# Kernel optimization log

Hardware: AMD Instinct MI355X
Metric: run time of the kernel (lower is better)

## Reference

```python
import jax, jax.numpy as jnp
import numpy as np
from jax import lax

B, KLEN, KDIM, QDIM, ADIM, VDIM = 32, 2000, 512, 512, 512, 512
CONV_CH, CONV_K = 10, 201

def setup_inputs() -> dict:
    key = jax.random.key(0)
    ks = jax.random.split(key, 16)
    s = lambda fan: 1.0 / np.sqrt(fan)
    return {
        "key": jax.random.normal(ks[0], (B, KLEN, KDIM), jnp.float32),
        "value": jax.random.normal(ks[1], (B, KLEN, VDIM), jnp.float32),
        "query": jax.random.normal(ks[2], (B, 1, QDIM), jnp.float32),
        "aw_prev": jnp.zeros((B, 1, KLEN), jnp.float32),
        "mask": jnp.ones((B, 1, KLEN), jnp.int32),
        # parameters (torch nn.Linear: y = x @ W.T + b, W is [out,in])
        "Wk": jax.random.uniform(ks[3], (ADIM, KDIM), jnp.float32, -s(KDIM), s(KDIM)),
        "bk": jax.random.uniform(ks[4], (ADIM,), jnp.float32, -s(KDIM), s(KDIM)),
        "Wq": jax.random.uniform(ks[5], (ADIM, QDIM), jnp.float32, -s(QDIM), s(QDIM)),
        "conv_w": jax.random.uniform(ks[6], (CONV_CH, 1, CONV_K), jnp.float32, -s(CONV_K), s(CONV_K)),
        "Wconv": jax.random.uniform(ks[7], (ADIM, CONV_CH), jnp.float32, -s(CONV_CH), s(CONV_CH)),
        "v": jax.random.uniform(ks[8], (ADIM,), jnp.float32, -s(ADIM), s(ADIM)),
    }

def reference(key, value, query, aw_prev, mask, Wk, bk, Wq, conv_w, Wconv, v):
    # location-aware attention, qlen == 1, sharpening_factor == 1, no dropout (eval)
    kproj = jnp.einsum('bkd,ad->bka', key, Wk) + bk              # [B, klen, adim]
    qproj = jnp.einsum('bqd,ad->bqa', query, Wq)                 # [B, 1, adim]
    # conv over previous attention weights: 1D 'same' conv, 1 -> CONV_CH channels
    conv_feat = lax.conv_general_dilated(
        aw_prev, conv_w, window_strides=(1,), padding='SAME',
        dimension_numbers=('NCH', 'OIH', 'NCH'))                 # [B, C, klen]
    conv_proj = jnp.einsum('bck,ac->bka', conv_feat, Wconv)      # [B, klen, adim]
    # additive score: v^T tanh(Wk k + Wq q + Wc f)
    tmp = jnp.tanh(kproj[:, None] + qproj[:, :, None] + conv_proj[:, None])  # [B,1,klen,adim]
    e = jnp.einsum('bqka,a->bqk', tmp, v)                        # [B, 1, klen]
    neg_inf = jnp.finfo(e.dtype).min
    e = jnp.where(mask == 0, neg_inf, e)
    aw = jax.nn.softmax(e, axis=-1)                              # [B, 1, klen]
    cv = jnp.einsum('bqk,bkv->bqv', aw, value)                   # [B, 1, vdim]
    return cv, aw[:, None]  # aw: [B, 1(H), 1(qlen), klen]
```

## Files before the change

### kernel.cpp

```cpp
#include <hip/hip_runtime.h>
#include <hip/hip_bf16.h>
#include <math.h>

#define B 32
#define KLEN 2000
#define KDIM 512
#define QDIM 512
#define ADIM 512
#define VDIM 512
#define CONV_CH 10
#define CONV_K 201
#define NROWS (B*KLEN)

#define NKS  33
#define ZERO16 {0,0,0,0,0,0,0,0,0,0,0,0,0,0,0,0}

#define NP_PACK 53
#define NP_QPRJ 26
#define NP_ZERO 26
#define NP_CONV 256

#define CH_LEN 63

typedef __attribute__((ext_vector_type(8)))  short bf16x8;
typedef __attribute__((ext_vector_type(16))) float f32x16;
typedef __attribute__((ext_vector_type(4)))  float f32x4;

__device__ __forceinline__ ushort f32_to_bf16(float f) {
    union { float f; unsigned int u; } v; v.f = f;
    unsigned int x = v.u;
    unsigned int r = (x + 0x7FFFu + ((x >> 16) & 1u)) >> 16;
    return (ushort)r;
}

__device__ __forceinline__ unsigned int pk_bf16(float lo, float hi) {
    union { __hip_bfloat162 h2; unsigned int u; } c;
    float2 t; t.x = lo; t.y = hi;
    c.h2 = __float22bfloat162_rn(t);
    return c.u;
}

__device__ __forceinline__ float fast_tanh(float x) {
    return 1.0f - 2.0f / (__expf(2.0f * x) + 1.0f);
}

#define MFMA32(a, bfr, c) __builtin_amdgcn_mfma_f32_32x32x16_bf16(a, bfr, c, 0, 0, 0)

__global__ __launch_bounds__(640, 2)
void k_prep(const float* __restrict__ Wk, const float* __restrict__ Wconv,
            const float* __restrict__ bk, ushort* __restrict__ wp,
            const float* __restrict__ query, const float* __restrict__ Wq,
            float* __restrict__ qproj,
            const float* __restrict__ aw_prev, const float* __restrict__ conv_w,
            float* __restrict__ cf, float* __restrict__ cv) {
    __shared__ float w_s[CONV_CH * 204];
    __shared__ float aw_s[464];
    const int bid = blockIdx.x, tid = threadIdx.x;

    if (bid < NP_PACK) {
        int t = bid * 640 + tid;
        if (t < 16 * NKS * 64) {
            int lane = t & 63;
            int idx = t >> 6;
            int ks = idx % NKS, nt = idx / NKS;
            int h = lane >> 5, r = lane & 31;
            int a = nt * 32 + r;
            int j0 = ks * 16 + h * 8;
            union { uint4 v; ushort u[8]; } pk;
            #pragma unroll
            for (int jj = 0; jj < 8; jj++) {
                int j = j0 + jj;
                float val;
                if (j < 512)       val = Wk[a * KDIM + j];
                else if (j < 522)  val = Wconv[a * CONV_CH + (j - 512)];
                else if (j == 522) val = bk[a];
                else               val = 0.f;
                pk.u[jj] = f32_to_bf16(val);
            }
            *(uint4*)(wp + (size_t)t * 8) = pk.v;
        }
    } else if (bid < NP_PACK + NP_QPRJ) {
        int t = (bid - NP_PACK) * 640 + tid;
        if (t < B * ADIM) {
            int b = t >> 9, a = t & 511;
            const f32x4* q = (const f32x4*)(query + b * QDIM);
            const f32x4* w = (const f32x4*)(Wq + a * QDIM);
            float acc = 0.f;
            #pragma unroll 4
            for (int i = 0; i < 128; i++) {
                f32x4 qv = q[i], wv = w[i];
                acc += qv[0]*wv[0] + qv[1]*wv[1] + qv[2]*wv[2] + qv[3]*wv[3];
            }
            qproj[t] = acc;
        }
    } else if (bid < NP_PACK + NP_QPRJ + NP_ZERO) {
        int t = (bid - NP_PACK - NP_QPRJ) * 640 + tid;
        if (t < B * VDIM) cv[t] = 0.f;
    } else {
        int cb = bid - NP_PACK - NP_QPRJ - NP_ZERO;
        int b = cb >> 3, chunk = cb & 7;
        int k0 = chunk * 256;
        for (int i = tid; i < CONV_CH * 204; i += 640) {
            int c = i / 204, t = i % 204;
            w_s[i] = (t < CONV_K) ? conv_w[c * CONV_K + t] : 0.f;
        }
        for (int i = tid; i < 464; i += 640) {
            int src = k0 - 100 + i;
            aw_s[i] = (src >= 0 && src < KLEN) ? aw_prev[b * KLEN + src] : 0.f;
        }
        __syncthreads();

        const int c = tid >> 6;
        const int k_local = (tid & 63) * 4;
        const float* wc = w_s + c * 204;
        float a0 = 0.f, a1 = 0.f, a2 = 0.f, a3 = 0.f;
        f32x4 r0 = *(const f32x4*)(aw_s + k_local);
        #pragma unroll 3
        for (int q = 0; q < 51; q++) {
            f32x4 r1 = *(const f32x4*)(aw_s + k_local + 4 * q + 4);
            float w0 = wc[4*q], w1 = wc[4*q+1], w2 = wc[4*q+2], w3 = wc[4*q+3];
            a0 += w0*r0[0]; a1 += w0*r0[1]; a2 += w0*r0[2]; a3 += w0*r0[3];
            a0 += w1*r0[1]; a1 += w1*r0[2]; a2 += w1*r0[3]; a3 += w1*r1[0];
            a0 += w2*r0[2]; a1 += w2*r0[3]; a2 += w2*r1[0]; a3 += w2*r1[1];
            a0 += w3*r0[3]; a1 += w3*r1[0]; a2 += w3*r1[1]; a3 += w3*r1[2];
            r0 = r1;
        }
        int k = k0 + k_local;
        float* dst = cf + ((size_t)b * CONV_CH + c) * KLEN + k;
        if (k + 3 < KLEN) {
            f32x4 o; o[0] = a0; o[1] = a1; o[2] = a2; o[3] = a3;
            *(f32x4*)dst = o;
        } else {
            if (k     < KLEN) dst[0] = a0;
            if (k + 1 < KLEN) dst[1] = a1;
            if (k + 2 < KLEN) dst[2] = a2;
            if (k + 3 < KLEN) dst[3] = a3;
        }
    }
}

__global__ __launch_bounds__(512, 4)
void k_main(const float* __restrict__ key, const ushort* __restrict__ wp,
            const float* __restrict__ qproj, const float* __restrict__ cf,
            const float* __restrict__ vvec, const int* __restrict__ mask,
            float* __restrict__ e_out) {
    __shared__ char Alds[65536];
    __shared__ float partsum[8][2][32];
    const int tid = threadIdx.x;
    const int wc = tid >> 6, lane = tid & 63;
    const int r = lane & 31, h = lane >> 5;
    const int b = blockIdx.x >> 5;
    const int kbase = (blockIdx.x & 31) * 64;

    #pragma unroll
    for (int i = 0; i < 8; i++) {
        int ch = tid + i * 512;
        int arow = ch >> 6, cx = ch & 63;
        int kpos = kbase + arow; if (kpos >= KLEN) kpos = KLEN - 1;
        const float* kp = key + ((size_t)b * KLEN + kpos) * KDIM + cx * 8;
        f32x4 f0 = __builtin_nontemporal_load((const f32x4*)kp);
        f32x4 f1 = __builtin_nontemporal_load((const f32x4*)(kp + 4));
        uint4 pk;
        pk.x = pk_bf16(f0[0], f0[1]);
        pk.y = pk_bf16(f0[2], f0[3]);
        pk.z = pk_bf16(f1[0], f1[1]);
        pk.w = pk_bf16(f1[2], f1[3]);
        int off = (arow << 10) + (cx << 4);
        off ^= (arow & 31) << 4;
        *(uint4*)(Alds + off) = pk;
    }
    __syncthreads();

    const ushort* bpW0 = wp + ((size_t)(wc * 2 + 0) * NKS * 64 + lane) * 8;
    const ushort* bpW1 = wp + ((size_t)(wc * 2 + 1) * NKS * 64 + lane) * 8;
    const int base_g0 = r * 1024 + h * 16;
    const int base_g1 = base_g0 + 32768;
    const int swz = r << 4;

    f32x16 c00 = ZERO16, c01 = ZERO16;
    f32x16 c10 = ZERO16, c11 = ZERO16;

    #pragma unroll 4
    for (int ks = 0; ks < 32; ks++) {
        bf16x8 k0 = *(const bf16x8*)(Alds + ((base_g0 + ks * 32) ^ swz));
        bf16x8 k1 = *(const bf16x8*)(Alds + ((base_g1 + ks * 32) ^ swz));
        bf16x8 w0 = *(const bf16x8*)(bpW0 + ks * 512);
        bf16x8 w1 = *(const bf16x8*)(bpW1 + ks * 512);
        c00 = MFMA32(w0, k0, c00); c01 = MFMA32(w0, k1, c01);
        c10 = MFMA32(w1, k0, c10); c11 = MFMA32(w1, k1, c11);
    }
    {
        auto build_ext = [&](int kpos) -> bf16x8 {
            int kc = kpos < KLEN ? kpos : KLEN - 1;
            const float* cfb = cf + ((size_t)b * CONV_CH) * KLEN + kc;
            union { bf16x8 v8; unsigned int u[4]; ushort us[8]; } pk;
            if (h == 0) {
                pk.u[0] = pk_bf16(cfb[0],              cfb[(size_t)1 * KLEN]);
                pk.u[1] = pk_bf16(cfb[(size_t)2*KLEN], cfb[(size_t)3 * KLEN]);
                pk.u[2] = pk_bf16(cfb[(size_t)4*KLEN], cfb[(size_t)5 * KLEN]);
                pk.u[3] = pk_bf16(cfb[(size_t)6*KLEN], cfb[(size_t)7 * KLEN]);
            } else {
                pk.u[0] = pk_bf16(cfb[(size_t)8*KLEN], cfb[(size_t)9 * KLEN]);
                pk.us[2] = 0x3F80;
                pk.us[3] = 0;
                pk.u[2] = 0; pk.u[3] = 0;
            }
            return pk.v8;
        };
        bf16x8 x0 = build_ext(kbase + r);
        bf16x8 x1 = build_ext(kbase + 32 + r);
        bf16x8 w0 = *(const bf16x8*)(bpW0 + 32 * 512);
        bf16x8 w1 = *(const bf16x8*)(bpW1 + 32 * 512);
        c00 = MFMA32(w0, x0, c00); c01 = MFMA32(w0, x1, c01);
        c10 = MFMA32(w1, x0, c10); c11 = MFMA32(w1, x1, c11);
    }

    const float* qb = qproj + b * ADIM + wc * 64;
    const float* vb = vvec + wc * 64;
    float pg0 = 0.f, pg1 = 0.f;
    #pragma unroll
    for (int t = 0; t < 2; t++) {
        const f32x16 a0 = t ? c10 : c00;
        const f32x16 a1 = t ? c11 : c01;
        #pragma unroll
        for (int q = 0; q < 4; q++) {
            f32x4 qv = *(const f32x4*)(qb + t * 32 + 8 * q + 4 * h);
            f32x4 vv = *(const f32x4*)(vb + t * 32 + 8 * q + 4 * h);
            #pragma unroll
            for (int j = 0; j < 4; j++) {
                int i = 4 * q + j;
                pg0 += fast_tanh(a0[i] + qv[j]) * vv[j];
                pg1 += fast_tanh(a1[i] + qv[j]) * vv[j];
            }
        }
    }
    pg0 += __shfl_xor(pg0, 32);
    pg1 += __shfl_xor(pg1, 32);
    if (h == 0) { partsum[wc][0][r] = pg0; partsum[wc][1][r] = pg1; }
    __syncthreads();

    if (tid < 64) {
        int g = tid >> 5, rr = tid & 31;
        float s = 0.f;
        #pragma unroll
        for (int w = 0; w < 8; w++) s += partsum[w][g][rr];
        int kpos = kbase + g * 32 + rr;
        if (kpos < KLEN) {
            int idx = b * KLEN + kpos;
            e_out[idx] = mask[idx] ? s : -3.4028235e38f;
        }
    }
}

__global__ __launch_bounds__(512, 4)
void k_cv(const float* __restrict__ e, const float* __restrict__ value,
          float* __restrict__ aw, float* __restrict__ cv) {
    int b = blockIdx.x >> 5, chunk = blockIdx.x & 31;
    const float* er = e + b * KLEN;
    __shared__ float redv[8];
    __shared__ float sa[CH_LEN + 1];
    __shared__ f32x4 red[3][128];
    int tid = threadIdx.x, lane = tid & 63, wv = tid >> 6;

    float m = -3.4028235e38f;
    for (int k = tid; k < KLEN; k += 512) m = fmaxf(m, er[k]);
    for (int o = 32; o; o >>= 1) m = fmaxf(m, __shfl_xor(m, o));
    if (lane == 0) redv[wv] = m;
    __syncthreads();
    m = fmaxf(fmaxf(fmaxf(redv[0], redv[1]), fmaxf(redv[2], redv[3])),
              fmaxf(fmaxf(redv[4], redv[5]), fmaxf(redv[6], redv[7])));
    __syncthreads();
    float s = 0.f;
    for (int k = tid; k < KLEN; k += 512) s += __expf(er[k] - m);
    for (int o = 32; o; o >>= 1) s += __shfl_xor(s, o);
    if (lane == 0) redv[wv] = s;
    __syncthreads();
    s = redv[0] + redv[1] + redv[2] + redv[3] + redv[4] + redv[5] + redv[6] + redv[7];
    const float inv = 1.0f / s;

    int k0 = chunk * CH_LEN;
    int len = KLEN - k0; if (len > CH_LEN) len = CH_LEN;
    if (tid < len) {
        float p = __expf(er[k0 + tid] - m) * inv;
        sa[tid] = p;
        aw[b * KLEN + k0 + tid] = p;
    }
    __syncthreads();

    const int kh = tid >> 7;
    const int colt = tid & 127;
    const float* vp = value + ((size_t)b * KLEN + k0) * VDIM + colt * 4;
    f32x4 acc = {0.f, 0.f, 0.f, 0.f};
    for (int k = kh; k < len; k += 4) {
        f32x4 vv = *(const f32x4*)(vp + (size_t)k * VDIM);
        acc += vv * sa[k];
    }
    if (kh) red[kh - 1][colt] = acc;
    __syncthreads();
    if (kh == 0) {
        acc += red[0][colt] + red[1][colt] + red[2][colt];
        float* dst = cv + b * VDIM + colt * 4;
        atomicAdd(dst + 0, acc[0]);
        atomicAdd(dst + 1, acc[1]);
        atomicAdd(dst + 2, acc[2]);
        atomicAdd(dst + 3, acc[3]);
    }
}

extern "C" void kernel_launch(void* const* d_in, const int* in_sizes, int n_in,
                              void* d_out, int out_size, void* d_ws, size_t ws_size,
                              hipStream_t stream) {
    const float* key     = (const float*)d_in[0];
    const float* value   = (const float*)d_in[1];
    const float* query   = (const float*)d_in[2];
    const float* aw_prev = (const float*)d_in[3];
    const int*   mask    = (const int*)d_in[4];
    const float* Wk      = (const float*)d_in[5];
    const float* bk      = (const float*)d_in[6];
    const float* Wq      = (const float*)d_in[7];
    const float* conv_w  = (const float*)d_in[8];
    const float* Wconv   = (const float*)d_in[9];
    const float* vvec    = (const float*)d_in[10];

    char* ws = (char*)d_ws;
    ushort* wp   = (ushort*)(ws + 0);
    float* qproj = (float*)(ws + 540672);
    float* cf    = (float*)(ws + 606208);
    float* e     = (float*)(ws + 3166208);

    float* cv = (float*)d_out;
    float* aw = (float*)d_out + B * VDIM;

    k_prep<<<NP_PACK + NP_QPRJ + NP_ZERO + NP_CONV, 640, 0, stream>>>(
              Wk, Wconv, bk, wp, query, Wq, qproj, aw_prev, conv_w, cf, cv);
    k_main<<<1024, 512, 0, stream>>>(key, wp, qproj, cf, vvec, mask, e);
    k_cv  <<<B*32, 512, 0, stream>>>(e, value, aw, cv);
}
```

Measured before the change: 140.2 us.

## Double k_main row tile to 128 keys per block to reuse weight fragments

```diff
diff --git a/kernel.cpp b/kernel.cpp
--- a/kernel.cpp
+++ b/kernel.cpp
@@ -139,27 +139,26 @@
     }
 }
 
-__global__ __launch_bounds__(512, 4)
+__global__ __launch_bounds__(512, 2)
 void k_main(const float* __restrict__ key, const ushort* __restrict__ wp,
             const float* __restrict__ qproj, const float* __restrict__ cf,
             const float* __restrict__ vvec, const int* __restrict__ mask,
             float* __restrict__ e_out) {
-    __shared__ char Alds[65536];
-    __shared__ float partsum[8][2][32];
+    __shared__ char Alds[131072];
     const int tid = threadIdx.x;
     const int wc = tid >> 6, lane = tid & 63;
     const int r = lane & 31, h = lane >> 5;
-    const int b = blockIdx.x >> 5;
-    const int kbase = (blockIdx.x & 31) * 64;
+    const int b = blockIdx.x >> 4;
+    const int kbase = (blockIdx.x & 15) * 128;
 
     #pragma unroll
-    for (int i = 0; i < 8; i++) {
+    for (int i = 0; i < 16; i++) {
         int ch = tid + i * 512;
         int arow = ch >> 6, cx = ch & 63;
         int kpos = kbase + arow; if (kpos >= KLEN) kpos = KLEN - 1;
         const float* kp = key + ((size_t)b * KLEN + kpos) * KDIM + cx * 8;
-        f32x4 f0 = __builtin_nontemporal_load((const f32x4*)kp);
-        f32x4 f1 = __builtin_nontemporal_load((const f32x4*)(kp + 4));
+        f32x4 f0 = *(const f32x4*)kp;
+        f32x4 f1 = *(const f32x4*)(kp + 4);
         uint4 pk;
         pk.x = pk_bf16(f0[0], f0[1]);
         pk.y = pk_bf16(f0[2], f0[3]);
@@ -173,21 +172,26 @@
 
     const ushort* bpW0 = wp + ((size_t)(wc * 2 + 0) * NKS * 64 + lane) * 8;
     const ushort* bpW1 = wp + ((size_t)(wc * 2 + 1) * NKS * 64 + lane) * 8;
-    const int base_g0 = r * 1024 + h * 16;
-    const int base_g1 = base_g0 + 32768;
+    const int koff = r * 1024 + h * 16;
     const int swz = r << 4;
 
     f32x16 c00 = ZERO16, c01 = ZERO16;
     f32x16 c10 = ZERO16, c11 = ZERO16;
-
-    #pragma unroll 4
+    f32x16 c20 = ZERO16, c21 = ZERO16;
+    f32x16 c30 = ZERO16, c31 = ZERO16;
+
+    #pragma unroll 2
     for (int ks = 0; ks < 32; ks++) {
-        bf16x8 k0 = *(const bf16x8*)(Alds + ((base_g0 + ks * 32) ^ swz));
-        bf16x8 k1 = *(const bf16x8*)(Alds + ((base_g1 + ks * 32) ^ swz));
+        bf16x8 k0 = *(const bf16x8*)(Alds + ((koff          + ks * 32) ^ swz));
+        bf16x8 k1 = *(const bf16x8*)(Alds + ((koff + 32768  + ks * 32) ^ swz));
+        bf16x8 k2 = *(const bf16x8*)(Alds + ((koff + 65536  + ks * 32) ^ swz));
+        bf16x8 k3 = *(const bf16x8*)(Alds + ((koff + 98304  + ks * 32) ^ swz));
         bf16x8 w0 = *(const bf16x8*)(bpW0 + ks * 512);
         bf16x8 w1 = *(const bf16x8*)(bpW1 + ks * 512);
-        c00 = MFMA32(w0, k0, c00); c01 = MFMA32(w0, k1, c01);
-        c10 = MFMA32(w1, k0, c10); c11 = MFMA32(w1, k1, c11);
+        c00 = MFMA32(w0, k0, c00); c10 = MFMA32(w0, k1, c10);
+        c20 = MFMA32(w0, k2, c20); c30 = MFMA32(w0, k3, c30);
+        c01 = MFMA32(w1, k0, c01); c11 = MFMA32(w1, k1, c11);
+        c21 = MFMA32(w1, k2, c21); c31 = MFMA32(w1, k3, c31);
     }
     {
         auto build_ext = [&](int kpos) -> bf16x8 {
@@ -209,41 +213,54 @@
         };
         bf16x8 x0 = build_ext(kbase + r);
         bf16x8 x1 = build_ext(kbase + 32 + r);
+        bf16x8 x2 = build_ext(kbase + 64 + r);
+        bf16x8 x3 = build_ext(kbase + 96 + r);
         bf16x8 w0 = *(const bf16x8*)(bpW0 + 32 * 512);
         bf16x8 w1 = *(const bf16x8*)(bpW1 + 32 * 512);
-        c00 = MFMA32(w0, x0, c00); c01 = MFMA32(w0, x1, c01);
-        c10 = MFMA32(w1, x0, c10); c11 = MFMA32(w1, x1, c11);
+        c00 = MFMA32(w0, x0, c00); c10 = MFMA32(w0, x1, c10);
+        c20 = MFMA32(w0, x2, c20); c30 = MFMA32(w0, x3, c30);
+        c01 = MFMA32(w1, x0, c01); c11 = MFMA32(w1, x1, c11);
+        c21 = MFMA32(w1, x2, c21); c31 = MFMA32(w1, x3, c31);
     }
 
     const float* qb = qproj + b * ADIM + wc * 64;
     const float* vb = vvec + wc * 64;
-    float pg0 = 0.f, pg1 = 0.f;
+    float pg0 = 0.f, pg1 = 0.f, pg2 = 0.f, pg3 = 0.f;
     #pragma unroll
-    for (int t = 0; t < 2; t++) {
-        const f32x16 a0 = t ? c10 : c00;
-        const f32x16 a1 = t ? c11 : c01;
+    for (int q = 0; q < 4; q++) {
+        f32x4 qv0 = *(const f32x4*)(qb + 8 * q + 4 * h);
+        f32x4 vv0 = *(const f32x4*)(vb + 8 * q + 4 * h);
+        f32x4 qv1 = *(const f32x4*)(qb + 32 + 8 * q + 4 * h);
+        f32x4 vv1 = *(const f32x4*)(vb + 32 + 8 * q + 4 * h);
         #pragma unroll
-        for (int q = 0; q < 4; q++) {
-            f32x4 qv = *(const f32x4*)(qb + t * 32 + 8 * q + 4 * h);
-            f32x4 vv = *(const f32x4*)(vb + t * 32 + 8 * q + 4 * h);
-            #pragma unroll
-            for (int j = 0; j < 4; j++) {
-                int i = 4 * q + j;
-                pg0 += fast_tanh(a0[i] + qv[j]) * vv[j];
-                pg1 += fast_tanh(a1[i] + qv[j]) * vv[j];
-            }
+        for (int j = 0; j < 4; j++) {
+            int i = 4 * q + j;
+            pg0 += fast_tanh(c00[i] + qv0[j]) * vv0[j] + fast_tanh(c01[i] + qv1[j]) * vv1[j];
+            pg1 += fast_tanh(c10[i] + qv0[j]) * vv0[j] + fast_tanh(c11[i] + qv1[j]) * vv1[j];
+            pg2 += fast_tanh(c20[i] + qv0[j]) * vv0[j] + fast_tanh(c21[i] + qv1[j]) * vv1[j];
+            pg3 += fast_tanh(c30[i] + qv0[j]) * vv0[j] + fast_tanh(c31[i] + qv1[j]) * vv1[j];
         }
     }
     pg0 += __shfl_xor(pg0, 32);
     pg1 += __shfl_xor(pg1, 32);
-    if (h == 0) { partsum[wc][0][r] = pg0; partsum[wc][1][r] = pg1; }
-    __syncthreads();
-
-    if (tid < 64) {
+    pg2 += __shfl_xor(pg2, 32);
+    pg3 += __shfl_xor(pg3, 32);
+
+    __syncthreads();
+    float* ps = (float*)Alds;
+    if (h == 0) {
+        ps[(wc * 4 + 0) * 32 + r] = pg0;
+        ps[(wc * 4 + 1) * 32 + r] = pg1;
+        ps[(wc * 4 + 2) * 32 + r] = pg2;
+        ps[(wc * 4 + 3) * 32 + r] = pg3;
+    }
+    __syncthreads();
+
+    if (tid < 128) {
         int g = tid >> 5, rr = tid & 31;
         float s = 0.f;
         #pragma unroll
-        for (int w = 0; w < 8; w++) s += partsum[w][g][rr];
+        for (int w = 0; w < 8; w++) s += ps[(w * 4 + g) * 32 + rr];
         int kpos = kbase + g * 32 + rr;
         if (kpos < KLEN) {
             int idx = b * KLEN + kpos;
@@ -333,6 +350,6 @@
 
     k_prep<<<NP_PACK + NP_QPRJ + NP_ZERO + NP_CONV, 640, 0, stream>>>(
               Wk, Wconv, bk, wp, query, Wq, qproj, aw_prev, conv_w, cf, cv);
-    k_main<<<1024, 512, 0, stream>>>(key, wp, qproj, cf, vvec, mask, e);
+    k_main<<<512, 512, 0, stream>>>(key, wp, qproj, cf, vvec, mask, e);
     k_cv  <<<B*32, 512, 0, stream>>>(e, value, aw, cv);
 }
```

Result: slower. 145.3 us (+3.6%).
